# Kernel optimization log

Hardware: AMD Instinct MI355X
Metric: run time of the kernel (lower is better)

The kernel has to match this reference:

```python
import jax, jax.numpy as jnp
import numpy as np

B, S, D = 4, 2048, 2048
NQ, NKV = 16, 4
HD = D // NQ          # head_size = 128
GROUP = NQ // NKV     # 4


def _rope_table(seq_len, head_size, theta=10000.0):
    # [seq, head_size/2, 2] = (cos, sin), matching torch polar freqs_cis
    inv = 1.0 / (theta ** (np.arange(0, head_size, 2, dtype=np.float32) / head_size))
    ang = np.arange(seq_len, dtype=np.float32)[:, None] * inv[None, :]
    return jnp.asarray(np.stack([np.cos(ang), np.sin(ang)], axis=-1))


def setup_inputs() -> dict:
    key = jax.random.key(0)
    ks = jax.random.split(key, 6)
    sd = 0.02
    return {
        "x": jax.random.normal(ks[0], (B, S, D), jnp.float32),
        "freq_cis": _rope_table(S, HD),
        "Wq": jax.random.normal(ks[1], (D, NQ * HD), jnp.float32) * sd,
        "bq": jnp.zeros((NQ * HD,), jnp.float32),
        "Wk": jax.random.normal(ks[2], (D, NKV * HD), jnp.float32) * sd,
        "bk": jnp.zeros((NKV * HD,), jnp.float32),
        "Wv": jax.random.normal(ks[3], (D, NKV * HD), jnp.float32) * sd,
        "bv": jnp.zeros((NKV * HD,), jnp.float32),
        "Wo": jax.random.normal(ks[4], (NQ * HD, D), jnp.float32) * sd,
        "start_pos": 0,
    }


def _apply_rope(x, fc):
    # x: [b, s, h, d]; fc: [s, d/2, 2] -> complex multiply on (even, odd) pairs
    xr = x.reshape(*x.shape[:-1], -1, 2)
    cos = fc[None, :, None, :, 0]
    sin = fc[None, :, None, :, 1]
    x0, x1 = xr[..., 0], xr[..., 1]
    out = jnp.stack([x0 * cos - x1 * sin, x0 * sin + x1 * cos], axis=-1)
    return out.reshape(x.shape)


def reference(x, freq_cis, Wq, bq, Wk, bk, Wv, bv, Wo, start_pos):
    b, s, _ = x.shape
    q = (x @ Wq + bq).reshape(b, s, NQ, HD)
    k = (x @ Wk + bk).reshape(b, s, NKV, HD)
    v = (x @ Wv + bv).reshape(b, s, NKV, HD)

    fc = freq_cis[start_pos:start_pos + s]
    q = _apply_rope(q, fc)
    k = _apply_rope(k, fc)

    # [b, nkv, group, s, d] query view; k/v stay [b, nkv, s, d] (GQA broadcast)
    q = q.transpose(0, 2, 1, 3).reshape(b, NKV, GROUP, s, HD)
    k = k.transpose(0, 2, 1, 3)
    v = v.transpose(0, 2, 1, 3)

    scale = 1.0 / jnp.sqrt(jnp.asarray(HD, x.dtype))
    scores = jnp.einsum("bhgqd,bhkd->bhgqk", q, k) * scale
    causal = jnp.tril(jnp.ones((s, s), bool))
    scores = jnp.where(causal[None, None, None], scores, jnp.asarray(-jnp.inf, scores.dtype))
    probs = jax.nn.softmax(scores, axis=-1)
    o = jnp.einsum("bhgqk,bhkd->bhgqd", probs, v)

    o = o.reshape(b, NQ, s, HD).transpose(0, 2, 1, 3).reshape(b, s, NQ * HD)
    return o @ Wo
```

## Files before the change

### kernel.cpp

```cpp
#include <hip/hip_runtime.h>
#include <stdint.h>

typedef __attribute__((ext_vector_type(8))) short bf16x8;
typedef __attribute__((ext_vector_type(4))) float f32x4;
typedef __attribute__((ext_vector_type(16))) float f32x16;

#define S_LEN 2048
#define D_MODEL 2048
#define NQH 16
#define NKVH 4
#define HDIM 128
#define BATCH 4

__device__ __forceinline__ float bf2f(unsigned short s) {
  union { unsigned u; float f; } v; v.u = ((unsigned)s) << 16; return v.f;
}
__device__ __forceinline__ unsigned short f2bf(float f) {
  union { float f; unsigned u; } v; v.f = f;
  unsigned r = v.u + 0x7FFFu + ((v.u >> 16) & 1u);
  return (unsigned short)(r >> 16);
}
__device__ __forceinline__ f32x4 fzero() {
  f32x4 v; v[0]=0.f; v[1]=0.f; v[2]=0.f; v[3]=0.f; return v;
}
__device__ __forceinline__ void async16(const void* g, void* l) {
  __builtin_amdgcn_global_load_lds(
      (const __attribute__((address_space(1))) unsigned int*)g,
      (__attribute__((address_space(3))) unsigned int*)l, 16, 0, 0);
}
__device__ __forceinline__ unsigned cvtpk(float lo, float hi) {
  unsigned r;
  asm("v_cvt_pk_bf16_f32 %0, %1, %2" : "=v"(r) : "v"(lo), "v"(hi));
  return r;
}

__global__ void k_convert_x(const float* __restrict__ x, unsigned short* __restrict__ xb, int n4) {
  int stride = gridDim.x * blockDim.x;
  for (int i = blockIdx.x * blockDim.x + threadIdx.x; i < n4; i += stride) {
    float4 v = ((const float4*)x)[i];
    ushort4 o;
    o.x = f2bf(v.x); o.y = f2bf(v.y); o.z = f2bf(v.z); o.w = f2bf(v.w);
    ((ushort4*)xb)[i] = o;
  }
}

__global__ void k_transpose_convert(const float* __restrict__ W, unsigned short* __restrict__ Wt,
                                    int K, int N) {
  __shared__ float tile[32][33];
  int tx = threadIdx.x & 31, ty = threadIdx.x >> 5;
  int n0 = blockIdx.x * 32, k0 = blockIdx.y * 32;
  #pragma unroll
  for (int i = 0; i < 4; ++i)
    tile[ty + i*8][tx] = W[(size_t)(k0 + ty + i*8) * N + n0 + tx];
  __syncthreads();
  #pragma unroll
  for (int i = 0; i < 4; ++i)
    Wt[(size_t)(n0 + ty + i*8) * K + k0 + tx] = f2bf(tile[tx][ty + i*8]);
}

__global__ void k_rope(unsigned short* __restrict__ T, const float* __restrict__ fc,
                       const int* __restrict__ start_pos, int total) {
  int sp = start_pos[0];
  int stride = gridDim.x * blockDim.x;
  for (int i = blockIdx.x * blockDim.x + threadIdx.x; i < total; i += stride) {
    int d2 = i & 63;
    int s = (i >> 6) & (S_LEN - 1);
    unsigned v = ((const unsigned*)T)[i];
    float x0 = bf2f((unsigned short)(v & 0xFFFFu));
    float x1 = bf2f((unsigned short)(v >> 16));
    float c  = fc[((size_t)(sp + s) * 64 + d2) * 2];
    float sn = fc[((size_t)(sp + s) * 64 + d2) * 2 + 1];
    float y0 = x0 * c - x1 * sn;
    float y1 = x0 * sn + x1 * c;
    ((unsigned*)T)[i] = (unsigned)f2bf(y0) | ((unsigned)f2bf(y1) << 16);
  }
}

#define BARRIER() __builtin_amdgcn_s_barrier()
#define LGKM0()  do { asm volatile("s_waitcnt lgkmcnt(0)" ::: "memory"); \
                      __builtin_amdgcn_sched_barrier(0); } while (0)
#define VMCNT6() asm volatile("s_waitcnt vmcnt(6)" ::: "memory")
#define VMCNT4() asm volatile("s_waitcnt vmcnt(4)" ::: "memory")
#define VMCNT0() asm volatile("s_waitcnt vmcnt(0)" ::: "memory")

__device__ __forceinline__ bf16x8 ldsrd(const unsigned short* L, int row, int kk, int g) {
  int Xs = (kk * 64 + g * 16) ^ ((row & 7) << 4);
  return *(const bf16x8*)&L[row * 64 + (Xs >> 1)];
}
__device__ __forceinline__ void stage8(const unsigned short* __restrict__ G, int gbase,
                                       int k0, unsigned short* lds, int rowbase, int lane) {
  int row = rowbase + (lane >> 3);
  int col8 = (lane & 7) ^ ((lane >> 3) & 7);
  async16(G + (size_t)(gbase + row) * 2048 + k0 + col8 * 8, lds + rowbase * 64 + lane * 8);
}

__global__ __launch_bounds__(512, 2) void k_gemm_qkv(
    const unsigned short* __restrict__ A, const unsigned short* __restrict__ Bt,
    const float* __restrict__ bq, const float* __restrict__ bk, const float* __restrict__ bv,
    unsigned short* __restrict__ Qo, unsigned short* __restrict__ Ko, unsigned short* __restrict__ Vto)
{
  __shared__ __align__(16) unsigned short Ab[3][256 * 64];
  __shared__ __align__(16) unsigned short Bb[3][128 * 64];
  const int NT = 32, NXT = 24;
  const int tid = threadIdx.x, lane = tid & 63, w = tid >> 6;
  const int lr = lane & 15, g = lane >> 4;
  const int wm = w >> 2, wn = w & 3;

  int nwg = NXT * 32;
  int cpx = nwg >> 3;
  int bid = blockIdx.x;
  int swz = (bid & 7) * cpx + (bid >> 3);
  const int by = swz / NXT, bx = swz % NXT;
  const int mbase = by * 256, nbase = bx * 128;

  #define ST_A(tt) { unsigned short* L = Ab[(tt) % 3]; int k0 = (tt) * 64; \
    _Pragma("unroll") for (int it = 0; it < 4; ++it) { int c = tid + it * 512; \
      int row = c >> 3, col8 = (c & 7) ^ (row & 7); \
      async16(A + (size_t)(mbase + row) * 2048 + k0 + col8 * 8, L + c * 8); } }
  #define ST_B(tt) { unsigned short* L = Bb[(tt) % 3]; int k0 = (tt) * 64; \
    _Pragma("unroll") for (int it = 0; it < 2; ++it) { int c = tid + it * 512; \
      int row = c >> 3, col8 = (c & 7) ^ (row & 7); \
      async16(Bt + (size_t)(nbase + row) * 2048 + k0 + col8 * 8, L + c * 8); } }

  f32x4 acc[8][2];
  #pragma unroll
  for (int m = 0; m < 8; ++m)
    #pragma unroll
    for (int n = 0; n < 2; ++n) acc[m][n] = fzero();

  ST_A(0); ST_B(0); ST_A(1); ST_B(1);
  VMCNT6();
  BARRIER();

  for (int t = 0; t < NT; ++t) {
    const unsigned short* Al = Ab[t % 3];
    const unsigned short* Bl = Bb[t % 3];
    bf16x8 a[2][4], b[2][2];

    #pragma unroll
    for (int kk = 0; kk < 2; ++kk) {
      #pragma unroll
      for (int m = 0; m < 4; ++m) a[kk][m] = ldsrd(Al, wm * 128 + m * 16 + lr, kk, g);
      #pragma unroll
      for (int n = 0; n < 2; ++n) b[kk][n] = ldsrd(Bl, wn * 32 + n * 16 + lr, kk, g);
    }
    if (t + 2 < NT) ST_A(t + 2);
    BARRIER(); LGKM0();
    __builtin_amdgcn_s_setprio(1);
    #pragma unroll
    for (int kk = 0; kk < 2; ++kk)
      #pragma unroll
      for (int m = 0; m < 4; ++m)
        #pragma unroll
        for (int n = 0; n < 2; ++n)
          acc[m][n] = __builtin_amdgcn_mfma_f32_16x16x32_bf16(a[kk][m], b[kk][n], acc[m][n], 0, 0, 0);
    __builtin_amdgcn_s_setprio(0);
    BARRIER();

    #pragma unroll
    for (int kk = 0; kk < 2; ++kk)
      #pragma unroll
      for (int m = 0; m < 4; ++m) a[kk][m] = ldsrd(Al, wm * 128 + 64 + m * 16 + lr, kk, g);
    if (t + 2 < NT) { ST_B(t + 2); VMCNT6(); } else { VMCNT0(); }
    BARRIER(); LGKM0();
    __builtin_amdgcn_s_setprio(1);
    #pragma unroll
    for (int kk = 0; kk < 2; ++kk)
      #pragma unroll
      for (int m = 0; m < 4; ++m)
        #pragma unroll
        for (int n = 0; n < 2; ++n)
          acc[4 + m][n] = __builtin_amdgcn_mfma_f32_16x16x32_bf16(a[kk][m], b[kk][n], acc[4 + m][n], 0, 0, 0);
    __builtin_amdgcn_s_setprio(0);
    BARRIER();
  }

  const float SCL2E = 0.08838834764831845f * 1.4426950408889634f;
  #pragma unroll
  for (int n = 0; n < 2; ++n) {
    const int ng = nbase + wn * 32 + n * 16 + lr;
    const int seg = (ng < 2048) ? 0 : (ng < 2560 ? 1 : 2);
    const int nn = ng - (seg == 0 ? 0 : (seg == 1 ? 2048 : 2560));
    const int hh = nn >> 7, dd = nn & 127;
    const float bias = (seg == 0 ? bq[nn] : (seg == 1 ? bk[nn] : bv[nn]));
    #pragma unroll
    for (int m = 0; m < 8; ++m)
      #pragma unroll
      for (int i = 0; i < 4; ++i) {
        int mg = mbase + wm * 128 + (m >> 2) * 64 + (m & 3) * 16 + g * 4 + i;
        int bb = mg >> 11, s = mg & 2047;
        float val = acc[m][n][i] + bias;
        if (seg == 0) {
          val *= SCL2E;
          Qo[((size_t)(bb * NQH + hh) * S_LEN + s) * HDIM + dd] = f2bf(val);
        } else if (seg == 1) {
          Ko[((size_t)(bb * NKVH + hh) * S_LEN + s) * HDIM + dd] = f2bf(val);
        } else {
          Vto[((size_t)(bb * NKVH + hh) * HDIM + dd) * S_LEN + s] = f2bf(val);
        }
      }
  }
  #undef ST_A
  #undef ST_B
}

__global__ __launch_bounds__(512, 2) void k_gemm_out256(
    const unsigned short* __restrict__ A, const unsigned short* __restrict__ Bt,
    float* __restrict__ Cf)
{
  __shared__ __align__(16) unsigned short Abuf[2][256 * 64];
  __shared__ __align__(16) unsigned short Bbuf[2][256 * 64];
  const int NT = 32, NXT = 8;
  const int tid = threadIdx.x, lane = tid & 63, w = tid >> 6;
  const int lr = lane & 15, g = lane >> 4;
  const int wm = w >> 2, wn = w & 3;

  int nwg = NXT * 32;
  int cpx = nwg >> 3;
  int bid = blockIdx.x;
  int swz = (bid & 7) * cpx + (bid >> 3);
  const int by = swz / NXT, bx = swz % NXT;
  const int mbase = by * 256, nbase = bx * 256;

  #define ST_AQ02(tt) if ((tt) < NT) { unsigned short* L = Abuf[(tt) & 1]; int k0 = (tt) * 64; \
    _Pragma("unroll") for (int it = 0; it < 2; ++it) { int sub = it * 8 + w; \
      stage8(A, mbase, k0, L, (sub >> 3) * 128 + (sub & 7) * 8, lane); } }
  #define ST_AQ13(tt) if ((tt) < NT) { unsigned short* L = Abuf[(tt) & 1]; int k0 = (tt) * 64; \
    _Pragma("unroll") for (int it = 0; it < 2; ++it) { int sub = it * 8 + w; \
      stage8(A, mbase, k0, L, 64 + (sub >> 3) * 128 + (sub & 7) * 8, lane); } }
  #define ST_BS0(tt) if ((tt) < NT) { unsigned short* L = Bbuf[(tt) & 1]; int k0 = (tt) * 64; \
    _Pragma("unroll") for (int it = 0; it < 2; ++it) { int sub = it * 8 + w; \
      stage8(Bt, nbase, k0, L, (sub >> 2) * 64 + (sub & 3) * 8, lane); } }
  #define ST_BS1(tt) if ((tt) < NT) { unsigned short* L = Bbuf[(tt) & 1]; int k0 = (tt) * 64; \
    _Pragma("unroll") for (int it = 0; it < 2; ++it) { int sub = it * 8 + w; \
      stage8(Bt, nbase, k0, L, 32 + (sub >> 2) * 64 + (sub & 3) * 8, lane); } }

  f32x4 acc[8][4];
  #pragma unroll
  for (int m = 0; m < 8; ++m)
    #pragma unroll
    for (int n = 0; n < 4; ++n) acc[m][n] = fzero();

  ST_AQ02(0); ST_AQ13(0); ST_BS0(0); ST_BS1(0);
  ST_AQ02(1); ST_BS1(1);
  VMCNT4();
  BARRIER();

  bf16x8 a[2][4], b[2][2];

  for (int t = 0; t < NT; ++t) {
    const unsigned short* Al = Abuf[t & 1];
    const unsigned short* Bl = Bbuf[t & 1];

    #pragma unroll
    for (int kk = 0; kk < 2; ++kk) {
      #pragma unroll
      for (int m = 0; m < 4; ++m) a[kk][m] = ldsrd(Al, wm * 128 + m * 16 + lr, kk, g);
      #pragma unroll
      for (int n = 0; n < 2; ++n) b[kk][n] = ldsrd(Bl, wn * 64 + n * 16 + lr, kk, g);
    }
    ST_AQ13(t + 1);
    BARRIER(); LGKM0();
    __builtin_amdgcn_s_setprio(1);
    #pragma unroll
    for (int kk = 0; kk < 2; ++kk)
      #pragma unroll
      for (int m = 0; m < 4; ++m)
        #pragma unroll
        for (int n = 0; n < 2; ++n)
          acc[m][n] = __builtin_amdgcn_mfma_f32_16x16x32_bf16(a[kk][m], b[kk][n], acc[m][n], 0, 0, 0);
    __builtin_amdgcn_s_setprio(0);
    BARRIER();

    #pragma unroll
    for (int kk = 0; kk < 2; ++kk)
      #pragma unroll
      for (int n = 0; n < 2; ++n) b[kk][n] = ldsrd(Bl, wn * 64 + (2 + n) * 16 + lr, kk, g);
    ST_BS0(t + 1);
    BARRIER(); LGKM0();
    __builtin_amdgcn_s_setprio(1);
    #pragma unroll
    for (int kk = 0; kk < 2; ++kk)
      #pragma unroll
      for (int m = 0; m < 4; ++m)
        #pragma unroll
        for (int n = 0; n < 2; ++n)
          acc[m][2 + n] = __builtin_amdgcn_mfma_f32_16x16x32_bf16(a[kk][m], b[kk][n], acc[m][2 + n], 0, 0, 0);
    __builtin_amdgcn_s_setprio(0);
    BARRIER();

    #pragma unroll
    for (int kk = 0; kk < 2; ++kk)
      #pragma unroll
      for (int m = 0; m < 4; ++m) a[kk][m] = ldsrd(Al, wm * 128 + 64 + m * 16 + lr, kk, g);
    ST_AQ02(t + 2);
    BARRIER(); LGKM0();
    __builtin_amdgcn_s_setprio(1);
    #pragma unroll
    for (int kk = 0; kk < 2; ++kk)
      #pragma unroll
      for (int m = 0; m < 4; ++m)
        #pragma unroll
        for (int n = 0; n < 2; ++n)
          acc[4 + m][2 + n] = __builtin_amdgcn_mfma_f32_16x16x32_bf16(a[kk][m], b[kk][n], acc[4 + m][2 + n], 0, 0, 0);
    __builtin_amdgcn_s_setprio(0);
    BARRIER();

    #pragma unroll
    for (int kk = 0; kk < 2; ++kk)
      #pragma unroll
      for (int n = 0; n < 2; ++n) b[kk][n] = ldsrd(Bl, wn * 64 + n * 16 + lr, kk, g);
    ST_BS1(t + 2);
    VMCNT4();
    BARRIER(); LGKM0();
    __builtin_amdgcn_s_setprio(1);
    #pragma unroll
    for (int kk = 0; kk < 2; ++kk)
      #pragma unroll
      for (int m = 0; m < 4; ++m)
        #pragma unroll
        for (int n = 0; n < 2; ++n)
          acc[4 + m][n] = __builtin_amdgcn_mfma_f32_16x16x32_bf16(a[kk][m], b[kk][n], acc[4 + m][n], 0, 0, 0);
    __builtin_amdgcn_s_setprio(0);
    BARRIER();
  }

  #pragma unroll
  for (int m = 0; m < 8; ++m)
    #pragma unroll
    for (int n = 0; n < 4; ++n)
      #pragma unroll
      for (int i = 0; i < 4; ++i) {
        int mg = mbase + wm * 128 + m * 16 + g * 4 + i;
        int ng = nbase + wn * 64 + n * 16 + lr;
        Cf[(size_t)mg * 2048 + ng] = acc[m][n][i];
      }
  #undef ST_AQ02
  #undef ST_AQ13
  #undef ST_BS0
  #undef ST_BS1
}

__global__ __launch_bounds__(512, 2) void k_flash2(
    const unsigned short* __restrict__ Q, const unsigned short* __restrict__ K,
    const unsigned short* __restrict__ Vt, unsigned short* __restrict__ O)
{
  __shared__ __align__(16) unsigned short SH[32768];

  const int tid = threadIdx.x;
  const int lane = tid & 63;
  const int w = tid >> 6;
  const int ql = lane & 31;
  const int hi = lane >> 5;

  const int bh = blockIdx.x >> 2;
  const int tp = blockIdx.x & 3;
  const int b = bh >> 4, h = bh & 15;
  const int kh = h >> 2;

  const unsigned short* Qbase = Q + (size_t)(b * NQH + h) * S_LEN * HDIM;
  const unsigned short* Kbase = K + (size_t)(b * NKVH + kh) * S_LEN * HDIM;
  const unsigned short* Vtb   = Vt + (size_t)(b * NKVH + kh) * HDIM * S_LEN;

  #pragma unroll 1
  for (int half = 0; half < 2; ++half) {
    const int t = half ? (7 - tp) : tp;
    const int nkv = 4 * t + 4;
    const int qg = t * 256 + w * 32 + ql;

    __syncthreads();

    bf16x8 qf[8];
    {
      const unsigned short* qp = Qbase + (size_t)qg * HDIM;
      #pragma unroll
      for (int dd = 0; dd < 8; ++dd)
        qf[dd] = *(const bf16x8*)(qp + dd * 16 + hi * 8);
    }

    float m_r = -1e30f, l_r = 0.f;
    f32x16 oA[4];
    #pragma unroll
    for (int db = 0; db < 4; ++db)
      #pragma unroll
      for (int r = 0; r < 16; ++r) oA[db][r] = 0.f;

    {
      unsigned short* Kd = SH;
      unsigned short* Vd = SH + 16384;
      #pragma unroll
      for (int it = 0; it < 2; ++it) {
        int c = tid + it * 512;
        int row = c >> 4, col = c & 15;
        int lcol = (col & 8) | ((col ^ (row & 7)) & 7);
        async16(Kbase + (size_t)row * HDIM + lcol * 8, Kd + c * 8);
      }
      #pragma unroll
      for (int it = 0; it < 2; ++it) {
        int c = tid + it * 512;
        int row = c >> 3, col = c & 7;
        int lcol = col ^ (row & 7);
        async16(Vtb + (size_t)row * S_LEN + lcol * 8, Vd + c * 8);
      }
    }
    __syncthreads();

    for (int j = 0; j < nkv; ++j) {
      const int cur = j & 1;
      const unsigned short* Kl = SH + cur * 8192;
      const unsigned short* Vl = SH + 16384 + cur * 8192;

      if (j + 1 < nkv) {
        unsigned short* Kd = SH + (cur ^ 1) * 8192;
        unsigned short* Vd = SH + 16384 + (cur ^ 1) * 8192;
        #pragma unroll
        for (int it = 0; it < 2; ++it) {
          int c = tid + it * 512;
          int row = c >> 4, col = c & 15;
          int lcol = (col & 8) | ((col ^ (row & 7)) & 7);
          async16(Kbase + (size_t)((j + 1) * 64 + row) * HDIM + lcol * 8, Kd + c * 8);
        }
        #pragma unroll
        for (int it = 0; it < 2; ++it) {
          int c = tid + it * 512;
          int row = c >> 3, col = c & 7;
          int lcol = col ^ (row & 7);
          async16(Vtb + (size_t)row * S_LEN + (j + 1) * 64 + lcol * 8, Vd + c * 8);
        }
      }

      if (j * 64 <= t * 256 + w * 32 + 31) {
        f32x16 p0, p1;
        #pragma unroll
        for (int r = 0; r < 16; ++r) { p0[r] = 0.f; p1[r] = 0.f; }
        #pragma unroll
        for (int dd = 0; dd < 8; ++dd) {
          const int off = (((dd * 32 + hi * 16) ^ ((ql & 7) << 4)) >> 1);
          bf16x8 a0 = *(const bf16x8*)&Kl[ql * 128 + off];
          bf16x8 a1 = *(const bf16x8*)&Kl[(32 + ql) * 128 + off];
          p0 = __builtin_amdgcn_mfma_f32_32x32x16_bf16(a0, qf[dd], p0, 0, 0, 0);
          p1 = __builtin_amdgcn_mfma_f32_32x32x16_bf16(a1, qf[dd], p1, 0, 0, 0);
        }

        #pragma unroll
        for (int r = 0; r < 16; ++r) {
          const int kl = (r & 3) + 8 * (r >> 2);
          int kg = j * 64 + kl + 4 * hi;
          if (kg > qg) p0[r] = -1e30f;
          if (kg + 32 > qg) p1[r] = -1e30f;
        }

        float pm = -1e30f;
        #pragma unroll
        for (int r = 0; r < 16; ++r) pm = fmaxf(pm, fmaxf(p0[r], p1[r]));
        pm = fmaxf(pm, __shfl_xor(pm, 32));
        if (!__all(pm - m_r <= 8.0f)) {
          const float mn = fmaxf(m_r, pm);
          const float corr = exp2f(m_r - mn);
          m_r = mn;
          l_r *= corr;
          #pragma unroll
          for (int db = 0; db < 4; ++db)
            #pragma unroll
            for (int r = 0; r < 16; ++r) oA[db][r] *= corr;
        }
        float rs = 0.f;
        #pragma unroll
        for (int r = 0; r < 16; ++r) {
          p0[r] = exp2f(p0[r] - m_r);
          p1[r] = exp2f(p1[r] - m_r);
          rs += p0[r] + p1[r];
        }
        rs += __shfl_xor(rs, 32);
        l_r += rs;

        bf16x8 pb[4];
        {
          unsigned Wv[8], W2v[8];
          #pragma unroll
          for (int d = 0; d < 4; ++d) {
            Wv[d]      = cvtpk(p0[4*d],     p0[4*d + 1]);
            W2v[d]     = cvtpk(p0[4*d + 2], p0[4*d + 3]);
            Wv[4 + d]  = cvtpk(p1[4*d],     p1[4*d + 1]);
            W2v[4 + d] = cvtpk(p1[4*d + 2], p1[4*d + 3]);
          }
          #pragma unroll
          for (int kt = 0; kt < 2; ++kt) {
            #pragma unroll
            for (int s = 0; s < 2; ++s) {
              unsigned ownW   = hi ? Wv[kt*4 + 2*s + 1]  : Wv[kt*4 + 2*s];
              unsigned sendW  = hi ? Wv[kt*4 + 2*s]      : Wv[kt*4 + 2*s + 1];
              unsigned recvW  = (unsigned)__shfl_xor((int)sendW, 32);
              unsigned ownW2  = hi ? W2v[kt*4 + 2*s + 1] : W2v[kt*4 + 2*s];
              unsigned sendW2 = hi ? W2v[kt*4 + 2*s]     : W2v[kt*4 + 2*s + 1];
              unsigned recvW2 = (unsigned)__shfl_xor((int)sendW2, 32);
              union { unsigned u[4]; bf16x8 v; } pk;
              pk.u[0] = hi ? recvW  : ownW;
              pk.u[1] = hi ? recvW2 : ownW2;
              pk.u[2] = hi ? ownW   : recvW;
              pk.u[3] = hi ? ownW2  : recvW2;
              pb[kt*2 + s] = pk.v;
            }
          }
        }

        #pragma unroll
        for (int ks = 0; ks < 4; ++ks) {
          #pragma unroll
          for (int db = 0; db < 4; ++db) {
            const int off = (((ks * 32 + hi * 16) ^ ((ql & 7) << 4)) >> 1);
            bf16x8 av = *(const bf16x8*)&Vl[(db * 32 + ql) * 64 + off];
            oA[db] = __builtin_amdgcn_mfma_f32_32x32x16_bf16(av, pb[ks], oA[db], 0, 0, 0);
          }
        }
      }
      __syncthreads();
    }

    {
      const float invl = 1.f / l_r;
      const int qloc = w * 32 + ql;
      #pragma unroll
      for (int db = 0; db < 4; ++db)
        #pragma unroll
        for (int g4 = 0; g4 < 4; ++g4) {
          unsigned lo  = cvtpk(oA[db][g4*4 + 0] * invl, oA[db][g4*4 + 1] * invl);
          unsigned hi2 = cvtpk(oA[db][g4*4 + 2] * invl, oA[db][g4*4 + 3] * invl);
          int byteoff = qloc * 256 + ((db * 64 + g4 * 16 + hi * 8) ^ ((qloc & 7) << 4));
          *(uint2*)((char*)SH + byteoff) = make_uint2(lo, hi2);
        }
    }
    __syncthreads();
    {
      const int q2 = tid >> 1, hf = tid & 1;
      unsigned short* orow = O + ((size_t)(b * S_LEN + t * 256 + q2)) * D_MODEL + h * HDIM + hf * 64;
      #pragma unroll
      for (int u = 0; u < 8; ++u) {
        int byteoff = q2 * 256 + ((hf * 128 + u * 16) ^ ((q2 & 7) << 4));
        bf16x8 v = *(const bf16x8*)((const char*)SH + byteoff);
        *(bf16x8*)(orow + u * 8) = v;
      }
    }
  }
}

extern "C" void kernel_launch(void* const* d_in, const int* in_sizes, int n_in,
                              void* d_out, int out_size, void* d_ws, size_t ws_size,
                              hipStream_t stream) {
  (void)in_sizes; (void)n_in; (void)out_size; (void)ws_size;
  const float* x  = (const float*)d_in[0];
  const float* fc = (const float*)d_in[1];
  const float* Wq = (const float*)d_in[2];
  const float* bq = (const float*)d_in[3];
  const float* Wk = (const float*)d_in[4];
  const float* bk = (const float*)d_in[5];
  const float* Wv = (const float*)d_in[6];
  const float* bv = (const float*)d_in[7];
  const float* Wo = (const float*)d_in[8];
  const int* start_pos = (const int*)d_in[9];
  float* out = (float*)d_out;

  unsigned short* ws = (unsigned short*)d_ws;
  size_t off = 0;
  unsigned short* xb  = ws + off; off += (size_t)8192 * 2048;
  unsigned short* Wt  = ws + off; off += (size_t)3072 * 2048;
  unsigned short* Wot = ws + off; off += (size_t)2048 * 2048;
  unsigned short* Qb  = ws + off; off += (size_t)BATCH * NQH  * S_LEN * HDIM;
  unsigned short* Kb  = ws + off; off += (size_t)BATCH * NKVH * S_LEN * HDIM;
  unsigned short* Vtb = ws + off; off += (size_t)BATCH * NKVH * S_LEN * HDIM;
  unsigned short* Ob  = ws + off; off += (size_t)8192 * 2048;

  k_convert_x<<<2048, 256, 0, stream>>>(x, xb, 8192 * 2048 / 4);
  k_transpose_convert<<<dim3(64, 64), 256, 0, stream>>>(Wq, Wt, 2048, 2048);
  k_transpose_convert<<<dim3(16, 64), 256, 0, stream>>>(Wk, Wt + (size_t)2048 * 2048, 2048, 512);
  k_transpose_convert<<<dim3(16, 64), 256, 0, stream>>>(Wv, Wt + (size_t)2560 * 2048, 2048, 512);
  k_transpose_convert<<<dim3(64, 64), 256, 0, stream>>>(Wo, Wot, 2048, 2048);

  k_gemm_qkv<<<dim3(768), 512, 0, stream>>>(xb, Wt, bq, bk, bv, Qb, Kb, Vtb);

  k_rope<<<2048, 256, 0, stream>>>(Qb, fc, start_pos, BATCH * NQH * S_LEN * 64);
  k_rope<<<2048, 256, 0, stream>>>(Kb, fc, start_pos, BATCH * NKVH * S_LEN * 64);

  k_flash2<<<dim3(256), 512, 0, stream>>>(Qb, Kb, Vtb, Ob);

  k_gemm_out256<<<dim3(256), 512, 0, stream>>>(Ob, Wot, out);
}
```

Measured before the change: 374.9 us.

## Merge prep launches, rebalance QKV GEMM warp tiling, triple-buffer flash KV loads

The four weight transpose launches become one kernel that dispatches on block index, and the two RoPE launches become one. The QKV GEMM warp layout changes from 2x4 to 4x2, so each warp owns a 64x64 tile and reloads B fragments instead of A between the two MFMA phases. The flash attention kernel moves from double to triple buffering of K/V tiles, waits on vmcnt instead of a full syncthreads, and raises wave priority around the MFMA blocks. This cuts launch overhead and is meant to hide global load latency, at the cost of more LDS per block in attention (96 KB), which may lower occupancy.

```diff
diff --git a/kernel.cpp b/kernel.cpp
--- a/kernel.cpp
+++ b/kernel.cpp
@@ -44,35 +44,45 @@
   }
 }
 
-__global__ void k_transpose_convert(const float* __restrict__ W, unsigned short* __restrict__ Wt,
-                                    int K, int N) {
+__global__ void k_transpose_all(const float* __restrict__ Wq, const float* __restrict__ Wk,
+                                const float* __restrict__ Wv, const float* __restrict__ Wo,
+                                unsigned short* __restrict__ Wt, unsigned short* __restrict__ Wot) {
   __shared__ float tile[32][33];
+  int bid = blockIdx.x;
+  const float* W; unsigned short* D; int N, nx;
+  if (bid < 4096)      { W = Wq; D = Wt;                          N = 2048; nx = 64; }
+  else if (bid < 5120) { W = Wk; D = Wt + (size_t)2048 * 2048;    N = 512;  nx = 16; bid -= 4096; }
+  else if (bid < 6144) { W = Wv; D = Wt + (size_t)2560 * 2048;    N = 512;  nx = 16; bid -= 5120; }
+  else                 { W = Wo; D = Wot;                         N = 2048; nx = 64; bid -= 6144; }
   int tx = threadIdx.x & 31, ty = threadIdx.x >> 5;
-  int n0 = blockIdx.x * 32, k0 = blockIdx.y * 32;
+  int n0 = (bid % nx) * 32, k0 = (bid / nx) * 32;
   #pragma unroll
   for (int i = 0; i < 4; ++i)
     tile[ty + i*8][tx] = W[(size_t)(k0 + ty + i*8) * N + n0 + tx];
   __syncthreads();
   #pragma unroll
   for (int i = 0; i < 4; ++i)
-    Wt[(size_t)(n0 + ty + i*8) * K + k0 + tx] = f2bf(tile[tx][ty + i*8]);
-}
-
-__global__ void k_rope(unsigned short* __restrict__ T, const float* __restrict__ fc,
-                       const int* __restrict__ start_pos, int total) {
+    D[(size_t)(n0 + ty + i*8) * 2048 + k0 + tx] = f2bf(tile[tx][ty + i*8]);
+}
+
+__global__ void k_rope2(unsigned short* __restrict__ Qb, unsigned short* __restrict__ Kb,
+                        const float* __restrict__ fc, const int* __restrict__ start_pos,
+                        int nq, int ntot) {
   int sp = start_pos[0];
   int stride = gridDim.x * blockDim.x;
-  for (int i = blockIdx.x * blockDim.x + threadIdx.x; i < total; i += stride) {
-    int d2 = i & 63;
-    int s = (i >> 6) & (S_LEN - 1);
-    unsigned v = ((const unsigned*)T)[i];
+  for (int i = blockIdx.x * blockDim.x + threadIdx.x; i < ntot; i += stride) {
+    unsigned* T = (i < nq) ? (unsigned*)Qb : (unsigned*)Kb;
+    int idx = (i < nq) ? i : i - nq;
+    int d2 = idx & 63;
+    int s = (idx >> 6) & (S_LEN - 1);
+    unsigned v = T[idx];
     float x0 = bf2f((unsigned short)(v & 0xFFFFu));
     float x1 = bf2f((unsigned short)(v >> 16));
     float c  = fc[((size_t)(sp + s) * 64 + d2) * 2];
     float sn = fc[((size_t)(sp + s) * 64 + d2) * 2 + 1];
     float y0 = x0 * c - x1 * sn;
     float y1 = x0 * sn + x1 * c;
-    ((unsigned*)T)[i] = (unsigned)f2bf(y0) | ((unsigned)f2bf(y1) << 16);
+    T[idx] = (unsigned)f2bf(y0) | ((unsigned)f2bf(y1) << 16);
   }
 }
 
@@ -104,7 +114,7 @@
   const int NT = 32, NXT = 24;
   const int tid = threadIdx.x, lane = tid & 63, w = tid >> 6;
   const int lr = lane & 15, g = lane >> 4;
-  const int wm = w >> 2, wn = w & 3;
+  const int wm = w >> 1, wn = w & 1;
 
   int nwg = NXT * 32;
   int cpx = nwg >> 3;
@@ -122,11 +132,11 @@
       int row = c >> 3, col8 = (c & 7) ^ (row & 7); \
       async16(Bt + (size_t)(nbase + row) * 2048 + k0 + col8 * 8, L + c * 8); } }
 
-  f32x4 acc[8][2];
+  f32x4 acc[4][4];
   #pragma unroll
-  for (int m = 0; m < 8; ++m)
-    #pragma unroll
-    for (int n = 0; n < 2; ++n) acc[m][n] = fzero();
+  for (int m = 0; m < 4; ++m)
+    #pragma unroll
+    for (int n = 0; n < 4; ++n) acc[m][n] = fzero();
 
   ST_A(0); ST_B(0); ST_A(1); ST_B(1);
   VMCNT6();
@@ -140,9 +150,9 @@
     #pragma unroll
     for (int kk = 0; kk < 2; ++kk) {
       #pragma unroll
-      for (int m = 0; m < 4; ++m) a[kk][m] = ldsrd(Al, wm * 128 + m * 16 + lr, kk, g);
-      #pragma unroll
-      for (int n = 0; n < 2; ++n) b[kk][n] = ldsrd(Bl, wn * 32 + n * 16 + lr, kk, g);
+      for (int m = 0; m < 4; ++m) a[kk][m] = ldsrd(Al, wm * 64 + m * 16 + lr, kk, g);
+      #pragma unroll
+      for (int n = 0; n < 2; ++n) b[kk][n] = ldsrd(Bl, wn * 64 + n * 16 + lr, kk, g);
     }
     if (t + 2 < NT) ST_A(t + 2);
     BARRIER(); LGKM0();
@@ -160,7 +170,7 @@
     #pragma unroll
     for (int kk = 0; kk < 2; ++kk)
       #pragma unroll
-      for (int m = 0; m < 4; ++m) a[kk][m] = ldsrd(Al, wm * 128 + 64 + m * 16 + lr, kk, g);
+      for (int n = 0; n < 2; ++n) b[kk][n] = ldsrd(Bl, wn * 64 + (2 + n) * 16 + lr, kk, g);
     if (t + 2 < NT) { ST_B(t + 2); VMCNT6(); } else { VMCNT0(); }
     BARRIER(); LGKM0();
     __builtin_amdgcn_s_setprio(1);
@@ -170,24 +180,24 @@
       for (int m = 0; m < 4; ++m)
         #pragma unroll
         for (int n = 0; n < 2; ++n)
-          acc[4 + m][n] = __builtin_amdgcn_mfma_f32_16x16x32_bf16(a[kk][m], b[kk][n], acc[4 + m][n], 0, 0, 0);
+          acc[m][2 + n] = __builtin_amdgcn_mfma_f32_16x16x32_bf16(a[kk][m], b[kk][n], acc[m][2 + n], 0, 0, 0);
     __builtin_amdgcn_s_setprio(0);
     BARRIER();
   }
 
   const float SCL2E = 0.08838834764831845f * 1.4426950408889634f;
   #pragma unroll
-  for (int n = 0; n < 2; ++n) {
-    const int ng = nbase + wn * 32 + n * 16 + lr;
+  for (int n = 0; n < 4; ++n) {
+    const int ng = nbase + wn * 64 + n * 16 + lr;
     const int seg = (ng < 2048) ? 0 : (ng < 2560 ? 1 : 2);
     const int nn = ng - (seg == 0 ? 0 : (seg == 1 ? 2048 : 2560));
     const int hh = nn >> 7, dd = nn & 127;
     const float bias = (seg == 0 ? bq[nn] : (seg == 1 ? bk[nn] : bv[nn]));
     #pragma unroll
-    for (int m = 0; m < 8; ++m)
+    for (int m = 0; m < 4; ++m)
       #pragma unroll
       for (int i = 0; i < 4; ++i) {
-        int mg = mbase + wm * 128 + (m >> 2) * 64 + (m & 3) * 16 + g * 4 + i;
+        int mg = mbase + wm * 64 + m * 16 + g * 4 + i;
         int bb = mg >> 11, s = mg & 2047;
         float val = acc[m][n][i] + bias;
         if (seg == 0) {
@@ -345,7 +355,7 @@
     const unsigned short* __restrict__ Q, const unsigned short* __restrict__ K,
     const unsigned short* __restrict__ Vt, unsigned short* __restrict__ O)
 {
-  __shared__ __align__(16) unsigned short SH[32768];
+  __shared__ __align__(16) unsigned short SH[49152];
 
   const int tid = threadIdx.x;
   const int lane = tid & 63;
@@ -362,6 +372,17 @@
   const unsigned short* Kbase = K + (size_t)(b * NKVH + kh) * S_LEN * HDIM;
   const unsigned short* Vtb   = Vt + (size_t)(b * NKVH + kh) * HDIM * S_LEN;
 
+  #define STAGEKV(jj) { unsigned short* Kd = SH + ((jj) % 3) * 16384; \
+    unsigned short* Vd = Kd + 8192; \
+    _Pragma("unroll") for (int it = 0; it < 2; ++it) { \
+      int c = tid + it * 512; int row = c >> 4, col = c & 15; \
+      int lcol = (col & 8) | ((col ^ (row & 7)) & 7); \
+      async16(Kbase + (size_t)((jj) * 64 + row) * HDIM + lcol * 8, Kd + c * 8); } \
+    _Pragma("unroll") for (int it = 0; it < 2; ++it) { \
+      int c = tid + it * 512; int row = c >> 3, col = c & 7; \
+      int lcol = col ^ (row & 7); \
+      async16(Vtb + (size_t)row * S_LEN + (jj) * 64 + lcol * 8, Vd + c * 8); } }
+
   #pragma unroll 1
   for (int half = 0; half < 2; ++half) {
     const int t = half ? (7 - tp) : tp;
@@ -385,54 +406,22 @@
       #pragma unroll
       for (int r = 0; r < 16; ++r) oA[db][r] = 0.f;
 
-    {
-      unsigned short* Kd = SH;
-      unsigned short* Vd = SH + 16384;
-      #pragma unroll
-      for (int it = 0; it < 2; ++it) {
-        int c = tid + it * 512;
-        int row = c >> 4, col = c & 15;
-        int lcol = (col & 8) | ((col ^ (row & 7)) & 7);
-        async16(Kbase + (size_t)row * HDIM + lcol * 8, Kd + c * 8);
-      }
-      #pragma unroll
-      for (int it = 0; it < 2; ++it) {
-        int c = tid + it * 512;
-        int row = c >> 3, col = c & 7;
-        int lcol = col ^ (row & 7);
-        async16(Vtb + (size_t)row * S_LEN + lcol * 8, Vd + c * 8);
-      }
-    }
-    __syncthreads();
+    STAGEKV(0);
+    STAGEKV(1);
+    VMCNT4();
+    BARRIER();
 
     for (int j = 0; j < nkv; ++j) {
-      const int cur = j & 1;
-      const unsigned short* Kl = SH + cur * 8192;
-      const unsigned short* Vl = SH + 16384 + cur * 8192;
-
-      if (j + 1 < nkv) {
-        unsigned short* Kd = SH + (cur ^ 1) * 8192;
-        unsigned short* Vd = SH + 16384 + (cur ^ 1) * 8192;
-        #pragma unroll
-        for (int it = 0; it < 2; ++it) {
-          int c = tid + it * 512;
-          int row = c >> 4, col = c & 15;
-          int lcol = (col & 8) | ((col ^ (row & 7)) & 7);
-          async16(Kbase + (size_t)((j + 1) * 64 + row) * HDIM + lcol * 8, Kd + c * 8);
-        }
-        #pragma unroll
-        for (int it = 0; it < 2; ++it) {
-          int c = tid + it * 512;
-          int row = c >> 3, col = c & 7;
-          int lcol = col ^ (row & 7);
-          async16(Vtb + (size_t)row * S_LEN + (j + 1) * 64 + lcol * 8, Vd + c * 8);
-        }
-      }
+      const unsigned short* Kl = SH + (j % 3) * 16384;
+      const unsigned short* Vl = Kl + 8192;
+
+      if (j + 2 < nkv) STAGEKV(j + 2);
 
       if (j * 64 <= t * 256 + w * 32 + 31) {
         f32x16 p0, p1;
         #pragma unroll
         for (int r = 0; r < 16; ++r) { p0[r] = 0.f; p1[r] = 0.f; }
+        __builtin_amdgcn_s_setprio(1);
         #pragma unroll
         for (int dd = 0; dd < 8; ++dd) {
           const int off = (((dd * 32 + hi * 16) ^ ((ql & 7) << 4)) >> 1);
@@ -441,6 +430,7 @@
           p0 = __builtin_amdgcn_mfma_f32_32x32x16_bf16(a0, qf[dd], p0, 0, 0, 0);
           p1 = __builtin_amdgcn_mfma_f32_32x32x16_bf16(a1, qf[dd], p1, 0, 0, 0);
         }
+        __builtin_amdgcn_s_setprio(0);
 
         #pragma unroll
         for (int r = 0; r < 16; ++r) {
@@ -504,6 +494,7 @@
           }
         }
 
+        __builtin_amdgcn_s_setprio(1);
         #pragma unroll
         for (int ks = 0; ks < 4; ++ks) {
           #pragma unroll
@@ -513,8 +504,12 @@
             oA[db] = __builtin_amdgcn_mfma_f32_32x32x16_bf16(av, pb[ks], oA[db], 0, 0, 0);
           }
         }
+        __builtin_amdgcn_s_setprio(0);
       }
-      __syncthreads();
+
+      if (j + 2 < nkv) { VMCNT4(); }
+      else if (j + 1 < nkv) { VMCNT0(); }
+      BARRIER();
     }
 
     {
@@ -542,6 +537,7 @@
       }
     }
   }
+  #undef STAGEKV
 }
 
 extern "C" void kernel_launch(void* const* d_in, const int* in_sizes, int n_in,
@@ -571,15 +567,13 @@
   unsigned short* Ob  = ws + off; off += (size_t)8192 * 2048;
 
   k_convert_x<<<2048, 256, 0, stream>>>(x, xb, 8192 * 2048 / 4);
-  k_transpose_convert<<<dim3(64, 64), 256, 0, stream>>>(Wq, Wt, 2048, 2048);
-  k_transpose_convert<<<dim3(16, 64), 256, 0, stream>>>(Wk, Wt + (size_t)2048 * 2048, 2048, 512);
-  k_transpose_convert<<<dim3(16, 64), 256, 0, stream>>>(Wv, Wt + (size_t)2560 * 2048, 2048, 512);
-  k_transpose_convert<<<dim3(64, 64), 256, 0, stream>>>(Wo, Wot, 2048, 2048);
+  k_transpose_all<<<10240, 256, 0, stream>>>(Wq, Wk, Wv, Wo, Wt, Wot);
 
   k_gemm_qkv<<<dim3(768), 512, 0, stream>>>(xb, Wt, bq, bk, bv, Qb, Kb, Vtb);
 
-  k_rope<<<2048, 256, 0, stream>>>(Qb, fc, start_pos, BATCH * NQH * S_LEN * 64);
-  k_rope<<<2048, 256, 0, stream>>>(Kb, fc, start_pos, BATCH * NKVH * S_LEN * 64);
+  k_rope2<<<2048, 256, 0, stream>>>(Qb, Kb, fc, start_pos,
+                                    BATCH * NQH * S_LEN * 64,
+                                    (BATCH * NQH + BATCH * NKVH) * S_LEN * 64);
 
   k_flash2<<<dim3(256), 512, 0, stream>>>(Qb, Kb, Vtb, Ob);
 
```

Result: no change. 373.6 us (-0.3%).
